# Kernel optimization log

Hardware: AMD Instinct MI355X
Metric: run time of the kernel (lower is better)

The kernel has to match this reference:

```python
import jax, jax.numpy as jnp
import numpy as np

PH = 8  # pool_height


def _box_grids(box, H, W, MW):
    """Replicates BidirectionalBoxPool._make_grid{_wide,_tall} + the flip.
    box: (4,) xyxy. Returns fwd grid (PH,MW,2), inverted grid (PH,MW,2), width."""
    xmin, ymin, xmax, ymax = box[0], box[1], box[2], box[3]
    bw = xmax - xmin
    bh = ymax - ymin
    is_zero = (xmin == 0) & (ymin == 0) & (xmax == 0) & (ymax == 0)
    wide = bw > bh
    den = jnp.where(wide, bh, bw)
    den = jnp.where(den == 0, 1.0, den)  # guard zero boxes
    ratio = jnp.where(wide, bw, bh) / den
    wf = jnp.ceil(ratio * PH)  # per-box width (float, used as int)
    wm1 = jnp.where(wf > 1, wf - 1.0, 1.0)
    each_w_wide = bw / wm1
    each_h_wide = bh / (PH - 1)
    each_w_tall = bh / wm1
    each_h_tall = bw / (PH - 1)
    halfW = W / 2.0
    halfH = H / 2.0

    def G(i, j):
        # wide: x follows j along box width, y follows i along pool height
        gx_w = (xmin + j * each_w_wide - halfW) / halfW
        gy_w = (ymin + i * each_h_wide - halfH) / halfH
        # tall (faithful to the original, including arange(height,0,-1)):
        gx_t = (xmin + i * each_h_tall - halfW) / halfW
        gy_t = ((wf - j) * each_w_tall + ymin - halfH) / halfH
        gx = jnp.broadcast_to(jnp.where(wide, gx_w, gx_t), (PH, MW))
        gy = jnp.broadcast_to(jnp.where(wide, gy_w, gy_t), (PH, MW))
        return jnp.stack([gx, gy], axis=-1)

    i = jnp.arange(PH, dtype=jnp.float32)[:, None]
    j = jnp.arange(MW, dtype=jnp.float32)[None, :]
    mask = jnp.broadcast_to((j < wf) & (~is_zero), (PH, MW))
    g_fwd = jnp.where(mask[..., None], G(i, j), -2.0)
    # grid.flip((0,1)) over the valid region == evaluate at flipped indices
    g_inv = jnp.where(mask[..., None], G(PH - 1.0 - i, wf - 1.0 - j), -2.0)
    w_out = jnp.where(is_zero, 0.0, wf)
    return g_fwd, g_inv, w_out


def _grid_sample(xf, grid, H, W):
    """F.grid_sample (bilinear, zeros padding, align_corners=False).
    xf: (C, H*W), grid: (Hg, Wg, 2) -> (C, Hg, Wg)."""
    ix = ((grid[..., 0] + 1.0) * W - 1.0) * 0.5
    iy = ((grid[..., 1] + 1.0) * H - 1.0) * 0.5
    x0 = jnp.floor(ix)
    y0 = jnp.floor(iy)
    out = jnp.zeros((xf.shape[0],) + grid.shape[:2], dtype=xf.dtype)
    for dx, dy in ((0, 0), (1, 0), (0, 1), (1, 1)):
        xi = x0 + dx
        yi = y0 + dy
        w = (1.0 - jnp.abs(ix - xi)) * (1.0 - jnp.abs(iy - yi))
        valid = (xi >= 0) & (xi < W) & (yi >= 0) & (yi < H)
        xi_c = jnp.clip(xi, 0, W - 1).astype(jnp.int32)
        yi_c = jnp.clip(yi, 0, H - 1).astype(jnp.int32)
        v = jnp.take(xf, yi_c * W + xi_c, axis=1)  # (C,Hg,Wg)
        out = out + v * (w * valid.astype(xf.dtype))[None, :, :]
    return out


def _forward(x, boxes, MW):
    N, C, H, W = x.shape
    B = boxes.shape[1]
    gf, gi, w = jax.vmap(jax.vmap(lambda b: _box_grids(b, H, W, MW)))(boxes)
    # (N, B, 2, PH, MW, 2) -> fold box/direction/row dims into sample rows
    grids = jnp.stack([gf, gi], axis=2).reshape(N, B * 2 * PH, MW, 2)
    xf = x.reshape(N, C, H * W)
    feats = jax.vmap(lambda xfn, gn: _grid_sample(xfn, gn, H, W))(xf, grids)
    feats = feats.reshape(N, C, B, 2, PH, MW).transpose(0, 2, 3, 1, 4, 5)
    widths = jnp.repeat(w[..., None], 2, axis=-1)  # (N,B,2)
    return feats, widths


def setup_inputs() -> dict:
    rng = np.random.default_rng(0)
    N, B, C, H, W = 8, 64, 32, 256, 256
    n_zero = 8
    short = rng.uniform(8.0, 32.0, (N, B))
    ratio = rng.uniform(1.5, 8.0, (N, B))
    long = short * ratio
    tall = rng.random((N, B)) < 0.5
    bw = np.where(tall, short, long)
    bh = np.where(tall, long, short)
    xmin = 1.0 + rng.random((N, B)) * (W - 2.0 - bw)
    ymin = 1.0 + rng.random((N, B)) * (H - 2.0 - bh)
    boxes = np.stack([xmin, ymin, xmin + bw, ymin + bh], axis=-1).astype(np.float32)
    boxes[:, -n_zero:, :] = 0.0  # zero boxes are skipped by the module
    # _max_width: ceil(max aspect ratio * pool_height); +1 slack for fp32 rounding
    max_width = int(np.ceil(ratio[:, :-n_zero].max() * PH)) + 1
    x = jax.random.normal(jax.random.key(0), (N, C, H, W), dtype=jnp.float32)
    return {"x": x, "boxes": jnp.asarray(boxes), "max_width": max_width}


def reference(x, boxes, max_width):
    return _forward(x, boxes, int(max_width))
```

## Files before the change

kernel.cpp:

```cpp
#include <hip/hip_runtime.h>

constexpr int N_  = 8;
constexpr int B_  = 64;
constexpr int C_  = 32;
constexpr int H_  = 256;
constexpr int W_  = 256;
constexpr int PH_ = 8;
constexpr int HW_ = H_ * W_;
constexpr int NB_ = N_ * B_;
constexpr int CPT_ = 8;
constexpr int CB_  = C_ / CPT_;

struct __attribute__((packed, aligned(4))) f2u { float a, b; };

__global__ __launch_bounds__(256)
void boxpool_v7(const float* __restrict__ x, const float* __restrict__ boxes,
                float* __restrict__ out, int MW, int PM, unsigned M16,
                int G, int pmb, long featsSize)
{
    const int Bx  = blockIdx.x;
    const int xcd = Bx & 7;
    const int s   = Bx >> 3;
    const int bq  = s / G;
    const int g   = s - bq * G;
    const int nb  = xcd * (NB_ / 8) + bq;
    const int cb  = g / pmb;
    const int pmblk = g - cb * pmb;
    const int tid = threadIdx.x;
    const int pm  = pmblk * 256 + tid;

    const float* bp = boxes + (long)nb * 4;
    const float xmin = bp[0], ymin = bp[1], xmax = bp[2], ymax = bp[3];
    const bool is_zero = (xmin == 0.f) && (ymin == 0.f) && (xmax == 0.f) && (ymax == 0.f);
    const float bw = xmax - xmin, bh = ymax - ymin;
    const bool wide = bw > bh;
    float den = wide ? bh : bw;
    den = (den == 0.f) ? 1.f : den;
    const float ratio = (wide ? bw : bh) / den;
    const float wf = ceilf(ratio * (float)PH_);
    const float wm1 = (wf > 1.f) ? (wf - 1.f) : 1.f;

    if (g == 0 && tid == 0) {
        float wv = is_zero ? 0.f : wf;
        out[featsSize + (long)nb * 2 + 0] = wv;
        out[featsSize + (long)nb * 2 + 1] = wv;
    }

    if (pm >= PM) return;

    const int i = (int)(((unsigned)pm * M16) >> 16);
    const int j = pm - i * MW;
    const int n = nb >> 6;
    const int c0 = cb * CPT_;

    const long obase = (long)nb * (2 * C_ * PM);
    float* o0p = out + obase + (long)c0 * PM + pm;

    const bool valid = !is_zero && ((float)j < wf);
    if (!valid) {
        float* o1p = out + obase + (long)(C_ + c0) * PM + pm;
        #pragma unroll
        for (int k = 0; k < CPT_; ++k) {
            o0p[(long)k * PM] = 0.f;
            o1p[(long)k * PM] = 0.f;
        }
        return;
    }

    const int i2 = (PH_ - 1) - i;
    const int j2 = (int)wf - 1 - j;
    float* o1p = out + obase + (long)(C_ + c0) * PM + (long)i2 * MW + j2;

    const float fi = (float)i, fj = (float)j;
    float xs, ys;
    if (wide) {
        xs = xmin + fj * (bw / wm1);
        ys = ymin + fi * (bh * (1.f / (float)(PH_ - 1)));
    } else {
        xs = xmin + fi * (bw * (1.f / (float)(PH_ - 1)));
        ys = ymin + (wf - fj) * (bh / wm1);
    }
    const float ix = xs - 0.5f;
    const float iy = ys - 0.5f;
    const float x0f = floorf(ix), y0f = floorf(iy);
    const int   x0  = (int)x0f,  y0  = (int)y0f;

    float wx1 = ix - x0f, wx0 = 1.f - wx1;
    float wy1 = iy - y0f, wy0 = 1.f - wy1;

    if (y0 < 0 || y0 >= H_)         wy0 = 0.f;
    if (y0 + 1 < 0 || y0 + 1 >= H_) wy1 = 0.f;
    const int y0c = min(max(y0, 0), H_ - 1);
    const int y1c = min(max(y0 + 1, 0), H_ - 1);

    if (x0 < 0 || x0 >= W_)         wx0 = 0.f;
    if (x0 + 1 < 0 || x0 + 1 >= W_) wx1 = 0.f;
    const int bx = min(max(x0, 0), W_ - 2);
    const float wl = (bx == x0) ? wx0 : ((bx == x0 + 1) ? wx1 : 0.f);
    const float wr = (bx + 1 == x0 + 1) ? wx1 : ((bx + 1 == x0) ? wx0 : 0.f);

    const int o0 = y0c * W_ + bx;
    const int o1 = y1c * W_ + bx;
    const float w00 = wl * wy0, w01 = wr * wy0;
    const float w10 = wl * wy1, w11 = wr * wy1;

    const float* xp = x + (long)(n * C_ + c0) * HW_;
    f2u r0[CPT_], r1[CPT_];
    #pragma unroll
    for (int k = 0; k < CPT_; ++k) {
        r0[k] = *reinterpret_cast<const f2u*>(xp + (long)k * HW_ + o0);
        r1[k] = *reinterpret_cast<const f2u*>(xp + (long)k * HW_ + o1);
    }
    __builtin_amdgcn_sched_barrier(0);

    #pragma unroll
    for (int k = 0; k < CPT_; ++k) {
        float v = w00 * r0[k].a + w01 * r0[k].b + w10 * r1[k].a + w11 * r1[k].b;
        o0p[(long)k * PM] = v;
        o1p[(long)k * PM] = v;
    }
}

extern "C" void kernel_launch(void* const* d_in, const int* in_sizes, int n_in,
                              void* d_out, int out_size, void* d_ws, size_t ws_size,
                              hipStream_t stream)
{
    const float* x     = (const float*)d_in[0];
    const float* boxes = (const float*)d_in[1];
    float* out = (float*)d_out;

    long total      = (long)out_size;
    long widthsSize = (long)N_ * B_ * 2;
    long featsSize  = total - widthsSize;
    int  MW         = (int)(featsSize / ((long)N_ * B_ * 2 * C_ * PH_));
    int  PM         = PH_ * MW;

    int pmb = (PM + 255) / 256;
    int G   = CB_ * pmb;
    int blocks = NB_ * G;

    unsigned M16 = (65536u + (unsigned)MW - 1u) / (unsigned)MW;

    hipLaunchKernelGGL(boxpool_v7, dim3(blocks), dim3(256), 0, stream,
                       x, boxes, out, MW, PM, M16, G, pmb, featsSize);
}
```

Measured before the change: 45.06 us.

## Split zero-fill of invalid tail into separate kernel, drop sched barrier

```diff
diff --git a/kernel.cpp b/kernel.cpp
--- a/kernel.cpp
+++ b/kernel.cpp
@@ -14,7 +14,38 @@
 struct __attribute__((packed, aligned(4))) f2u { float a, b; };
 
 __global__ __launch_bounds__(256)
-void boxpool_v7(const float* __restrict__ x, const float* __restrict__ boxes,
+void zerofill_tail(const float* __restrict__ boxes, float* __restrict__ out,
+                   int MW, int PM)
+{
+    const int nb = blockIdx.x;
+    const float* bp = boxes + (long)nb * 4;
+    const float xmin = bp[0], ymin = bp[1], xmax = bp[2], ymax = bp[3];
+    const bool is_zero = (xmin == 0.f) && (ymin == 0.f) && (xmax == 0.f) && (ymax == 0.f);
+    const float bw = xmax - xmin, bh = ymax - ymin;
+    const bool wide = bw > bh;
+    float den = wide ? bh : bw;
+    den = (den == 0.f) ? 1.f : den;
+    const float ratio = (wide ? bw : bh) / den;
+    const float wf = ceilf(ratio * (float)PH_);
+
+    const int start = is_zero ? 0 : (int)wf;
+    const int L = MW - start;
+    if (L <= 0) return;
+
+    const int wave = threadIdx.x >> 6;
+    const int lane = threadIdx.x & 63;
+    const long base0 = (long)nb * (2 * C_ * PM);
+
+    for (int r = wave; r < 2 * C_ * PH_; r += 4) {
+        const int dc = r >> 3;
+        const int i  = r & 7;
+        float* p = out + base0 + (long)dc * PM + i * MW + start;
+        for (int off = lane; off < L; off += 64) p[off] = 0.f;
+    }
+}
+
+__global__ __launch_bounds__(256)
+void boxpool_v9(const float* __restrict__ x, const float* __restrict__ boxes,
                 float* __restrict__ out, int MW, int PM, unsigned M16,
                 int G, int pmb, long featsSize)
 {
@@ -46,27 +77,17 @@
         out[featsSize + (long)nb * 2 + 1] = wv;
     }
 
-    if (pm >= PM) return;
+    if (pm >= PM || is_zero) return;
 
     const int i = (int)(((unsigned)pm * M16) >> 16);
     const int j = pm - i * MW;
+    if ((float)j >= wf) return;
+
     const int n = nb >> 6;
     const int c0 = cb * CPT_;
 
     const long obase = (long)nb * (2 * C_ * PM);
     float* o0p = out + obase + (long)c0 * PM + pm;
-
-    const bool valid = !is_zero && ((float)j < wf);
-    if (!valid) {
-        float* o1p = out + obase + (long)(C_ + c0) * PM + pm;
-        #pragma unroll
-        for (int k = 0; k < CPT_; ++k) {
-            o0p[(long)k * PM] = 0.f;
-            o1p[(long)k * PM] = 0.f;
-        }
-        return;
-    }
-
     const int i2 = (PH_ - 1) - i;
     const int j2 = (int)wf - 1 - j;
     float* o1p = out + obase + (long)(C_ + c0) * PM + (long)i2 * MW + j2;
@@ -111,8 +132,6 @@
         r0[k] = *reinterpret_cast<const f2u*>(xp + (long)k * HW_ + o0);
         r1[k] = *reinterpret_cast<const f2u*>(xp + (long)k * HW_ + o1);
     }
-    __builtin_amdgcn_sched_barrier(0);
-
     #pragma unroll
     for (int k = 0; k < CPT_; ++k) {
         float v = w00 * r0[k].a + w01 * r0[k].b + w10 * r1[k].a + w11 * r1[k].b;
@@ -141,6 +160,8 @@
 
     unsigned M16 = (65536u + (unsigned)MW - 1u) / (unsigned)MW;
 
-    hipLaunchKernelGGL(boxpool_v7, dim3(blocks), dim3(256), 0, stream,
+    hipLaunchKernelGGL(zerofill_tail, dim3(NB_), dim3(256), 0, stream,
+                       boxes, out, MW, PM);
+    hipLaunchKernelGGL(boxpool_v9, dim3(blocks), dim3(256), 0, stream,
                        x, boxes, out, MW, PM, M16, G, pmb, featsSize);
 }
```

Result: slower. 67.47 us (+49.7%).

## Stage box ROI into LDS per channel with double-buffered async loads

Applied to the files above, without the earlier changes.

```diff
diff --git a/kernel.cpp b/kernel.cpp
--- a/kernel.cpp
+++ b/kernel.cpp
@@ -8,26 +8,26 @@
 constexpr int PH_ = 8;
 constexpr int HW_ = H_ * W_;
 constexpr int NB_ = N_ * B_;
-constexpr int CPT_ = 8;
-constexpr int CB_  = C_ / CPT_;
+constexpr int GCH_ = 16;
+constexpr int CAP_ = 8960;
 
-struct __attribute__((packed, aligned(4))) f2u { float a, b; };
+__global__ __launch_bounds__(1024)
+void boxpool_v10(const float* __restrict__ x, const float* __restrict__ boxes,
+                 float* __restrict__ out, int MW, int PM, unsigned M16,
+                 long featsSize)
+{
+    __shared__ float roi[2][CAP_];
 
-__global__ __launch_bounds__(256)
-void boxpool_v7(const float* __restrict__ x, const float* __restrict__ boxes,
-                float* __restrict__ out, int MW, int PM, unsigned M16,
-                int G, int pmb, long featsSize)
-{
     const int Bx  = blockIdx.x;
     const int xcd = Bx & 7;
     const int s   = Bx >> 3;
-    const int bq  = s / G;
-    const int g   = s - bq * G;
-    const int nb  = xcd * (NB_ / 8) + bq;
-    const int cb  = g / pmb;
-    const int pmblk = g - cb * pmb;
+    const int nb  = xcd * 64 + (s >> 1);
+    const int grp = s & 1;
+    const int c0  = grp * GCH_;
     const int tid = threadIdx.x;
-    const int pm  = pmblk * 256 + tid;
+    const int wid = tid >> 6;
+    const int lane = tid & 63;
+    const int n   = nb >> 6;
 
     const float* bp = boxes + (long)nb * 4;
     const float xmin = bp[0], ymin = bp[1], xmax = bp[2], ymax = bp[3];
@@ -40,84 +40,110 @@
     const float wf = ceilf(ratio * (float)PH_);
     const float wm1 = (wf > 1.f) ? (wf - 1.f) : 1.f;
 
-    if (g == 0 && tid == 0) {
+    if (grp == 0 && tid == 0) {
         float wv = is_zero ? 0.f : wf;
         out[featsSize + (long)nb * 2 + 0] = wv;
         out[featsSize + (long)nb * 2 + 1] = wv;
     }
 
-    if (pm >= PM) return;
+    float ysmin, ysmax;
+    if (wide) { ysmin = ymin; ysmax = ymin + bh; }
+    else      { float e = bh / wm1; ysmin = ymin + e; ysmax = ymin + wf * e; }
+    const int gx0 = min(max((int)floorf(xmin - 0.5f), 0), W_ - 1);
+    const int gx1 = min(max((int)floorf(xmin + bw - 0.5f) + 1, 0), W_ - 1);
+    const int gy0 = min(max((int)floorf(ysmin - 0.5f), 0), H_ - 1);
+    const int gy1 = min(max((int)floorf(ysmax - 0.5f) + 1, 0), H_ - 1);
+    const int rw  = gx1 - gx0 + 1;
+    int rh  = gy1 - gy0 + 1;
+    const int rwp = (rw & 1) ? rw : rw + 1;
+    if ((long)rh * rwp > CAP_) rh = CAP_ / rwp;
 
-    const int i = (int)(((unsigned)pm * M16) >> 16);
-    const int j = pm - i * MW;
-    const int n = nb >> 6;
-    const int c0 = cb * CPT_;
+    const int npts = PH_ * MW;
+    float W00[2], W01[2], W10[2], W11[2];
+    int   O00[2], O10[2], OFF1[2];
+    bool  INR[2], VALv[2];
+    #pragma unroll
+    for (int sp = 0; sp < 2; ++sp) {
+        const int p = tid + sp * 1024;
+        const bool inr = p < npts;
+        INR[sp] = inr;
+        const int pp = inr ? p : 0;
+        const int i = (int)(((unsigned)pp * M16) >> 16);
+        const int j = pp - i * MW;
+        const bool valid = inr && !is_zero && ((float)j < wf);
+        VALv[sp] = valid;
 
-    const long obase = (long)nb * (2 * C_ * PM);
-    float* o0p = out + obase + (long)c0 * PM + pm;
+        const float fi = (float)i, fj = (float)j;
+        float xs, ys;
+        if (wide) { xs = xmin + fj * (bw / wm1); ys = ymin + fi * (bh * (1.f / 7.f)); }
+        else      { xs = xmin + fi * (bw * (1.f / 7.f)); ys = ymin + (wf - fj) * (bh / wm1); }
+        const float ix = xs - 0.5f, iy = ys - 0.5f;
+        const float x0f = floorf(ix), y0f = floorf(iy);
+        const int x0 = (int)x0f, y0 = (int)y0f;
 
-    const bool valid = !is_zero && ((float)j < wf);
-    if (!valid) {
-        float* o1p = out + obase + (long)(C_ + c0) * PM + pm;
-        #pragma unroll
-        for (int k = 0; k < CPT_; ++k) {
-            o0p[(long)k * PM] = 0.f;
-            o1p[(long)k * PM] = 0.f;
-        }
-        return;
+        float wx1 = ix - x0f, wx0 = 1.f - wx1;
+        float wy1 = iy - y0f, wy0 = 1.f - wy1;
+        if (y0 < 0 || y0 >= H_)         wy0 = 0.f;
+        if (y0 + 1 < 0 || y0 + 1 >= H_) wy1 = 0.f;
+        const int y0c = min(max(y0, 0), H_ - 1);
+        const int y1c = min(max(y0 + 1, 0), H_ - 1);
+        if (x0 < 0 || x0 >= W_)         wx0 = 0.f;
+        if (x0 + 1 < 0 || x0 + 1 >= W_) wx1 = 0.f;
+        const int bx = min(max(x0, 0), W_ - 2);
+        const float wl = (bx == x0) ? wx0 : ((bx == x0 + 1) ? wx1 : 0.f);
+        const float wr = (bx + 1 == x0 + 1) ? wx1 : ((bx + 1 == x0) ? wx0 : 0.f);
+
+        const int xl  = min(max(bx - gx0, 0), max(rw - 2, 0));
+        const int y0l = min(max(y0c - gy0, 0), rh - 1);
+        const int y1l = min(max(y1c - gy0, 0), rh - 1);
+
+        W00[sp] = wl * wy0; W01[sp] = wr * wy0;
+        W10[sp] = wl * wy1; W11[sp] = wr * wy1;
+        O00[sp] = y0l * rwp + xl;
+        O10[sp] = y1l * rwp + xl;
+        const int i2 = (PH_ - 1) - i;
+        const int j2 = (int)wf - 1 - j;
+        OFF1[sp] = valid ? (i2 * MW + j2) : pp;
     }
 
-    const int i2 = (PH_ - 1) - i;
-    const int j2 = (int)wf - 1 - j;
-    float* o1p = out + obase + (long)(C_ + c0) * PM + (long)i2 * MW + j2;
+    auto stage = [&](int c, int buf) {
+        if (is_zero) return;
+        const float* plane = x + (long)(n * C_ + c0 + c) * HW_;
+        for (int r = wid; r < rh; r += 16) {
+            const float* grow = plane + (gy0 + r) * W_ + gx0;
+            float* lrow = &roi[buf][r * rwp];
+            for (int cc = 0; cc < rw; cc += 64) {
+                if (cc + lane < rw) {
+                    __builtin_amdgcn_global_load_lds(
+                        (const __attribute__((address_space(1))) unsigned int*)(grow + cc + lane),
+                        (__attribute__((address_space(3))) unsigned int*)(lrow + cc),
+                        4, 0, 0);
+                }
+            }
+        }
+    };
 
-    const float fi = (float)i, fj = (float)j;
-    float xs, ys;
-    if (wide) {
-        xs = xmin + fj * (bw / wm1);
-        ys = ymin + fi * (bh * (1.f / (float)(PH_ - 1)));
-    } else {
-        xs = xmin + fi * (bw * (1.f / (float)(PH_ - 1)));
-        ys = ymin + (wf - fj) * (bh / wm1);
-    }
-    const float ix = xs - 0.5f;
-    const float iy = ys - 0.5f;
-    const float x0f = floorf(ix), y0f = floorf(iy);
-    const int   x0  = (int)x0f,  y0  = (int)y0f;
+    stage(0, 0);
+    __syncthreads();
 
-    float wx1 = ix - x0f, wx0 = 1.f - wx1;
-    float wy1 = iy - y0f, wy0 = 1.f - wy1;
-
-    if (y0 < 0 || y0 >= H_)         wy0 = 0.f;
-    if (y0 + 1 < 0 || y0 + 1 >= H_) wy1 = 0.f;
-    const int y0c = min(max(y0, 0), H_ - 1);
-    const int y1c = min(max(y0 + 1, 0), H_ - 1);
-
-    if (x0 < 0 || x0 >= W_)         wx0 = 0.f;
-    if (x0 + 1 < 0 || x0 + 1 >= W_) wx1 = 0.f;
-    const int bx = min(max(x0, 0), W_ - 2);
-    const float wl = (bx == x0) ? wx0 : ((bx == x0 + 1) ? wx1 : 0.f);
-    const float wr = (bx + 1 == x0 + 1) ? wx1 : ((bx + 1 == x0) ? wx0 : 0.f);
-
-    const int o0 = y0c * W_ + bx;
-    const int o1 = y1c * W_ + bx;
-    const float w00 = wl * wy0, w01 = wr * wy0;
-    const float w10 = wl * wy1, w11 = wr * wy1;
-
-    const float* xp = x + (long)(n * C_ + c0) * HW_;
-    f2u r0[CPT_], r1[CPT_];
-    #pragma unroll
-    for (int k = 0; k < CPT_; ++k) {
-        r0[k] = *reinterpret_cast<const f2u*>(xp + (long)k * HW_ + o0);
-        r1[k] = *reinterpret_cast<const f2u*>(xp + (long)k * HW_ + o1);
-    }
-    __builtin_amdgcn_sched_barrier(0);
-
-    #pragma unroll
-    for (int k = 0; k < CPT_; ++k) {
-        float v = w00 * r0[k].a + w01 * r0[k].b + w10 * r1[k].a + w11 * r1[k].b;
-        o0p[(long)k * PM] = v;
-        o1p[(long)k * PM] = v;
+    float* obase = out + (long)nb * (2 * C_ * PM) + (long)c0 * PM;
+    for (int c = 0; c < GCH_; ++c) {
+        if (c + 1 < GCH_) stage(c + 1, (c + 1) & 1);
+        const float* bc = roi[c & 1];
+        float* ob = obase + (long)c * PM;
+        #pragma unroll
+        for (int sp = 0; sp < 2; ++sp) {
+            if (!INR[sp]) continue;
+            float v = 0.f;
+            if (VALv[sp]) {
+                v = W00[sp] * bc[O00[sp]] + W01[sp] * bc[O00[sp] + 1]
+                  + W10[sp] * bc[O10[sp]] + W11[sp] * bc[O10[sp] + 1];
+            }
+            const int p = tid + sp * 1024;
+            ob[p] = v;
+            ob[(long)C_ * PM + OFF1[sp]] = v;
+        }
+        __syncthreads();
     }
 }
 
@@ -135,12 +161,8 @@
     int  MW         = (int)(featsSize / ((long)N_ * B_ * 2 * C_ * PH_));
     int  PM         = PH_ * MW;
 
-    int pmb = (PM + 255) / 256;
-    int G   = CB_ * pmb;
-    int blocks = NB_ * G;
-
     unsigned M16 = (65536u + (unsigned)MW - 1u) / (unsigned)MW;
 
-    hipLaunchKernelGGL(boxpool_v7, dim3(blocks), dim3(256), 0, stream,
-                       x, boxes, out, MW, PM, M16, G, pmb, featsSize);
+    hipLaunchKernelGGL(boxpool_v10, dim3(NB_ * 2), dim3(1024), 0, stream,
+                       x, boxes, out, MW, PM, M16, featsSize);
 }
```

Result: slower. 68.78 us (+52.6%).
